# Optimization experiments

Measured on AMD Instinct MI355X. Metric: run time of the kernel, lower is better.

## Reference

```python
import jax, jax.numpy as jnp
import numpy as np

H_DIM = 1024
HEAD_SIZE = 1024


def setup_inputs() -> dict:
    key = jax.random.key(0)
    ks = jax.random.split(key, 7)
    s = 1.0 / np.sqrt(H_DIM)
    x = jax.random.normal(ks[0], (4, 4096, H_DIM), dtype=jnp.float32)
    Wq = jax.random.uniform(ks[1], (H_DIM, HEAD_SIZE), jnp.float32, -s, s)
    bq = jax.random.uniform(ks[2], (HEAD_SIZE,), jnp.float32, -s, s)
    Wk = jax.random.uniform(ks[3], (H_DIM, HEAD_SIZE), jnp.float32, -s, s)
    bk = jax.random.uniform(ks[4], (HEAD_SIZE,), jnp.float32, -s, s)
    Wv = jax.random.uniform(ks[5], (H_DIM, HEAD_SIZE), jnp.float32, -s, s)
    bv = jax.random.uniform(ks[6], (HEAD_SIZE,), jnp.float32, -s, s)
    return {"x": x, "Wq": Wq, "bq": bq, "Wk": Wk, "bk": bk, "Wv": Wv, "bv": bv}


def reference(x, Wq, bq, Wk, bk, Wv, bv):
    B, S, _ = x.shape
    q = x @ Wq + bq  # [B,S,hs]
    k = x @ Wk + bk
    v = x @ Wv + bv
    scores = jnp.einsum('bqd,bkd->bqk', q, k)  # [B,S,S]
    causal = jnp.tril(jnp.ones((S, S), dtype=bool))
    scores = jnp.where(causal, scores, -jnp.inf)
    # original divides after masking; -inf stays -inf so math is identical
    w = jax.nn.softmax(scores / jnp.sqrt(jnp.float32(HEAD_SIZE)), axis=-1)
    # dropout p=0.0 -> identity
    return jnp.einsum('bqk,bkd->bqd', w, v)
```

## Files before the change

kernel.cpp:

```cpp
#include <hip/hip_runtime.h>
#include <stdint.h>

typedef _Float16 f16;
typedef _Float16 v8h __attribute__((ext_vector_type(8)));
typedef _Float16 v4h __attribute__((ext_vector_type(4)));
typedef float v4f __attribute__((ext_vector_type(4)));

#define LOG2E 1.44269504088896340736f
#define PT 16384

__device__ __forceinline__ void gll16(const void* g, void* l) {
  __builtin_amdgcn_global_load_lds((__attribute__((address_space(1))) void*)g,
                                   (__attribute__((address_space(3))) void*)l,
                                   16, 0, 0);
}

__device__ __forceinline__ int xcd_swz(int p, int chunk) {
  return (p & 7) * chunk + (p >> 3);
}

__global__ void k_cvt_x(const float* __restrict__ x, f16* __restrict__ xh, int n4) {
  int i = blockIdx.x * blockDim.x + threadIdx.x;
  if (i >= n4) return;
  float4 v = ((const float4*)x)[i];
  v4h o;
  o[0] = (f16)v.x; o[1] = (f16)v.y; o[2] = (f16)v.z; o[3] = (f16)v.w;
  ((v4h*)xh)[i] = o;
}

__global__ void k_cvt_wt(const float* __restrict__ Wq, const float* __restrict__ Wk,
                         const float* __restrict__ Wv, f16* __restrict__ Wt) {
  __shared__ f16 tile[64][65];
  int z = blockIdx.z;
  const float* W = (z == 0) ? Wq : (z == 1) ? Wk : Wv;
  int k0 = blockIdx.y * 64, n0 = blockIdx.x * 64;
  int t = threadIdx.x;
  int r = t >> 4, c4 = t & 15;
  for (int i = 0; i < 4; ++i) {
    int row = r + i * 16;
    float4 v = *(const float4*)&W[(size_t)(k0 + row) * 1024 + n0 + c4 * 4];
    tile[c4 * 4 + 0][row] = (f16)v.x;
    tile[c4 * 4 + 1][row] = (f16)v.y;
    tile[c4 * 4 + 2][row] = (f16)v.z;
    tile[c4 * 4 + 3][row] = (f16)v.w;
  }
  __syncthreads();
  f16* out = Wt + (size_t)z * 1048576;
  for (int i = 0; i < 4; ++i) {
    int n = r + i * 16;
    v4h o;
    o[0] = tile[n][c4 * 4 + 0];
    o[1] = tile[n][c4 * 4 + 1];
    o[2] = tile[n][c4 * 4 + 2];
    o[3] = tile[n][c4 * 4 + 3];
    *(v4h*)&out[(size_t)(n0 + n) * 1024 + k0 + c4 * 4] = o;
  }
}

__global__ __launch_bounds__(512) void k_qkv(
    const f16* __restrict__ xh,
    const f16* __restrict__ Wt,
    const float* __restrict__ bq, const float* __restrict__ bk, const float* __restrict__ bv,
    f16* __restrict__ q, f16* __restrict__ k, f16* __restrict__ vT) {
  __shared__ __align__(16) f16 As[2][16384];
  __shared__ __align__(16) f16 Bs[2][16384];
  int p = blockIdx.x + 64 * (blockIdx.y + 4 * blockIdx.z);
  int l = xcd_swz(p, 96);
  int mt = l / 12;
  int rem = l - mt * 12;
  int z = rem >> 2, nt = rem & 3;
  int m0 = mt * 256, n0 = nt * 256;
  const f16* gA = xh + (size_t)m0 * 1024;
  const f16* gB = Wt + (size_t)z * 1048576 + (size_t)n0 * 1024;
  const float* bias = (z == 0) ? bq : (z == 1) ? bk : bv;
  int tid = threadIdx.x;
  int lane = tid & 63, wave = tid >> 6;
  int quad = lane >> 4, l15 = lane & 15;
  int wm = (wave >> 2) * 128, wn = (wave & 3) * 64;

  int soff[4], slds[4];
#pragma unroll
  for (int h = 0; h < 4; ++h) {
    int s = h * 512 + tid;
    int row = s >> 3;
    int c = (s & 7) ^ (row & 7);
    soff[h] = row * 1024 + c * 8;
    slds[h] = (h * 512 + wave * 64) * 8;
  }
  v4f acc[8][4] = {};
  v8h a[8], bfr[4];

#define QSTAGE(dst, g, kf) do {                                            \
    _Pragma("unroll") for (int h = 0; h < 4; ++h)                          \
      gll16((g) + soff[h] + (kf), &(dst)[slds[h]]);                        \
  } while (0)

#define QREAD(d, ks) do {                                                  \
    int sl = (((ks) * 4 + quad) ^ (l15 & 7)) * 8;                          \
    _Pragma("unroll") for (int i = 0; i < 8; ++i)                          \
      a[i] = *(const v8h*)&As[d][(wm + i * 16 + l15) * 64 + sl];           \
    _Pragma("unroll") for (int j = 0; j < 4; ++j)                          \
      bfr[j] = *(const v8h*)&Bs[d][(wn + j * 16 + l15) * 64 + sl];         \
  } while (0)

#define QMFMA() do {                                                       \
    __builtin_amdgcn_s_setprio(1);                                         \
    _Pragma("unroll") for (int i = 0; i < 8; ++i)                          \
      _Pragma("unroll") for (int j = 0; j < 4; ++j)                        \
        acc[i][j] = __builtin_amdgcn_mfma_f32_16x16x32_f16(a[i], bfr[j], acc[i][j], 0, 0, 0); \
    __builtin_amdgcn_s_setprio(0);                                         \
  } while (0)

  QSTAGE(As[0], gA, 0);
  QSTAGE(Bs[0], gB, 0);

#pragma unroll 1
  for (int it = 0; it < 7; ++it) {
    int k1 = (2 * it + 1) * 64, k2 = (2 * it + 2) * 64;
    QSTAGE(As[1], gA, k1);
    asm volatile("s_waitcnt vmcnt(4)" ::: "memory");
    __builtin_amdgcn_s_barrier();
    QREAD(0, 0); QMFMA();
    QREAD(0, 1);
    QSTAGE(Bs[1], gB, k1);
    QMFMA();
    __builtin_amdgcn_s_barrier();
    QSTAGE(As[0], gA, k2);
    asm volatile("s_waitcnt vmcnt(4)" ::: "memory");
    __builtin_amdgcn_s_barrier();
    QREAD(1, 0); QMFMA();
    QREAD(1, 1);
    QSTAGE(Bs[0], gB, k2);
    QMFMA();
    __builtin_amdgcn_s_barrier();
  }
  {
    int k1 = 15 * 64;
    QSTAGE(As[1], gA, k1);
    asm volatile("s_waitcnt vmcnt(4)" ::: "memory");
    __builtin_amdgcn_s_barrier();
    QREAD(0, 0); QMFMA();
    QREAD(0, 1);
    QSTAGE(Bs[1], gB, k1);
    QMFMA();
    __builtin_amdgcn_s_barrier();
    asm volatile("s_waitcnt vmcnt(0)" ::: "memory");
    __builtin_amdgcn_s_barrier();
    QREAD(1, 0); QMFMA();
    QREAD(1, 1); QMFMA();
  }
#undef QSTAGE
#undef QREAD
#undef QMFMA

  if (z < 2) {
    f16* outp = (z == 0) ? q : k;
    float scale = (z == 0) ? 0.03125f : 1.0f;
#pragma unroll
    for (int j = 0; j < 4; ++j) {
      int n = n0 + wn + j * 16 + l15;
      float bia = bias[n];
#pragma unroll
      for (int i = 0; i < 8; ++i) {
        int mb = m0 + wm + i * 16 + quad * 4;
#pragma unroll
        for (int r = 0; r < 4; ++r)
          outp[(size_t)(mb + r) * 1024 + n] = (f16)((acc[i][j][r] + bia) * scale);
      }
    }
  } else {
#pragma unroll
    for (int j = 0; j < 4; ++j) {
      int n = n0 + wn + j * 16 + l15;
      float bia = bias[n];
#pragma unroll
      for (int i = 0; i < 8; ++i) {
        int m = m0 + wm + i * 16 + quad * 4;
        int bb = m >> 12, s = m & 4095;
        v4h o;
#pragma unroll
        for (int r = 0; r < 4; ++r) o[r] = (f16)(acc[i][j][r] + bia);
        *(v4h*)&vT[((size_t)bb * 1024 + n) * 4096 + s] = o;
      }
    }
  }
}

__global__ void k_zero(float* __restrict__ p) {
  p[blockIdx.x * 256 + threadIdx.x] = 0.f;
}

__global__ __launch_bounds__(256) void k_sgemm(
    const f16* __restrict__ q, const f16* __restrict__ kmat,
    f16* __restrict__ P, float* __restrict__ rowsum, int b0) {
  __shared__ __align__(16) f16 As[128 * 32];
  __shared__ __align__(16) f16 Bs[128 * 32];
  int p = blockIdx.x + 528 * blockIdx.y;
  int l = xcd_swz(p, 132);
  int i = (l >= 528) ? l - 528 : l;
  int bb = (l >= 528) ? 1 : 0;
  int b = b0 * 2 + bb;
  int mt = (int)((sqrtf(8.f * i + 1.f) - 1.f) * 0.5f);
  while ((mt + 1) * (mt + 2) / 2 <= i) ++mt;
  while (mt * (mt + 1) / 2 > i) --mt;
  int nt = i - mt * (mt + 1) / 2;
  const f16* A = q + ((size_t)b * 4096 + (size_t)mt * 128) * 1024;
  const f16* B = kmat + ((size_t)b * 4096 + (size_t)nt * 128) * 1024;
  f16* Pt = P + (size_t)bb * 528 * PT + (size_t)i * PT;

  int tid = threadIdx.x;
  int lane = tid & 63, wave = tid >> 6;
  int quad = lane >> 4, l15 = lane & 15;
  int wm = (wave & 1) * 64, wn = (wave >> 1) * 64;
  v4f acc[4][4] = {};

  for (int kk = 0; kk < 1024; kk += 32) {
    __syncthreads();
    for (int h = 0; h < 2; ++h) {
      int s = h * 256 + tid;
      int row = s >> 2, pos = s & 3;
      int c = pos ^ (row & 3);
      gll16(&A[(size_t)row * 1024 + kk + c * 8], &As[(h * 256 + wave * 64) * 8]);
    }
    for (int h = 0; h < 2; ++h) {
      int s = h * 256 + tid;
      int row = s >> 2, pos = s & 3;
      int c = pos ^ (row & 3);
      gll16(&B[(size_t)row * 1024 + kk + c * 8], &Bs[(h * 256 + wave * 64) * 8]);
    }
    __syncthreads();
    v8h a[4], bf[4];
    for (int ii = 0; ii < 4; ++ii) {
      int rowa = wm + ii * 16 + l15;
      int pa = quad ^ (rowa & 3);
      a[ii] = *(const v8h*)&As[rowa * 32 + pa * 8];
      int rowb = wn + ii * 16 + l15;
      int pb = quad ^ (rowb & 3);
      bf[ii] = *(const v8h*)&Bs[rowb * 32 + pb * 8];
    }
    for (int ii = 0; ii < 4; ++ii)
      for (int j = 0; j < 4; ++j)
        acc[ii][j] = __builtin_amdgcn_mfma_f32_16x16x32_f16(a[ii], bf[j], acc[ii][j], 0, 0, 0);
  }

  bool diag = (nt == mt);
  float* rsb = rowsum + (size_t)b * 4096 + mt * 128;
  for (int ii = 0; ii < 4; ++ii) {
    int rl = wm + ii * 16 + quad * 4;
    for (int r = 0; r < 4; ++r) {
      int row_l = rl + r;
      float rs = 0.f;
      for (int j = 0; j < 4; ++j) {
        int col_l = wn + j * 16 + l15;
        float pv = __builtin_amdgcn_exp2f(acc[ii][j][r] * LOG2E);
        if (diag && col_l > row_l) pv = 0.f;
        Pt[(size_t)row_l * 128 + col_l] = (f16)pv;
        rs += pv;
      }
      rs += __shfl_xor(rs, 1, 64);
      rs += __shfl_xor(rs, 2, 64);
      rs += __shfl_xor(rs, 4, 64);
      rs += __shfl_xor(rs, 8, 64);
      if (l15 == 0) atomicAdd(&rsb[row_l], rs);
    }
  }
}

__global__ __launch_bounds__(256) void k_pv(
    const f16* __restrict__ P, const f16* __restrict__ vT,
    const float* __restrict__ rowsum, float* __restrict__ out, int b0) {
  __shared__ __align__(16) f16 As[2][8192];
  __shared__ __align__(16) f16 Bs[2][4096];
  int p = blockIdx.x + 16 * (blockIdx.y + 16 * blockIdx.z);
  int l = xcd_swz(p, 64);
  int dt = l & 15;
  int pr = (l >> 4) & 15;
  int bb = l >> 8;
  int b = b0 * 2 + bb;
  const f16* Pb = P + (size_t)bb * 528 * PT;
  const f16* Vb = vT + (size_t)b * 1024 * 4096;
  int tid = threadIdx.x;
  int lane = tid & 63, wave = tid >> 6;
  int quad = lane >> 4, l15 = lane & 15;
  int wm = (wave & 1) * 64, wn = (wave >> 1) * 32;

  int aoff[4], aslds[4];
#pragma unroll
  for (int h = 0; h < 4; ++h) {
    int s = h * 256 + tid;
    int row = s >> 3;
    int c = (s & 7) ^ (row & 7);
    aoff[h] = row * 128 + c * 8;
    aslds[h] = (h * 256 + wave * 64) * 8;
  }
  int boff[2], bslds[2];
#pragma unroll
  for (int h = 0; h < 2; ++h) {
    int s = h * 256 + tid;
    int row = s >> 3;
    int c = (s & 7) ^ (row & 7);
    boff[h] = (dt * 64 + row) * 4096 + c * 8;
    bslds[h] = (h * 256 + wave * 64) * 8;
  }
  v8h a[4], b_[2];

#define PSTAGE_A(d, Pt_, kc) do {                                          \
    _Pragma("unroll") for (int h = 0; h < 4; ++h)                          \
      gll16((Pt_) + aoff[h] + (kc), &As[d][aslds[h]]);                     \
  } while (0)
#define PSTAGE_B(d, koff) do {                                             \
    _Pragma("unroll") for (int h = 0; h < 2; ++h)                          \
      gll16(Vb + boff[h] + (koff), &Bs[d][bslds[h]]);                      \
  } while (0)
#define PREAD(d, ks) do {                                                  \
    int sl = (((ks) * 4 + quad) ^ (l15 & 7)) * 8;                          \
    _Pragma("unroll") for (int ii = 0; ii < 4; ++ii)                       \
      a[ii] = *(const v8h*)&As[d][(wm + ii * 16 + l15) * 64 + sl];         \
    _Pragma("unroll") for (int j = 0; j < 2; ++j)                          \
      b_[j] = *(const v8h*)&Bs[d][(wn + j * 16 + l15) * 64 + sl];          \
  } while (0)
#define PMFMA(acc_) do {                                                   \
    __builtin_amdgcn_s_setprio(1);                                         \
    _Pragma("unroll") for (int ii = 0; ii < 4; ++ii)                       \
      _Pragma("unroll") for (int j = 0; j < 2; ++j)                        \
        acc_[ii][j] = __builtin_amdgcn_mfma_f32_16x16x32_f16(a[ii], b_[j], acc_[ii][j], 0, 0, 0); \
    __builtin_amdgcn_s_setprio(0);                                         \
  } while (0)

  for (int half = 0; half < 2; ++half) {
    int mt = half ? (31 - pr) : pr;
    size_t ptri = (size_t)mt * (mt + 1) / 2;
    v4f acc[4][2] = {};
    PSTAGE_A(0, Pb + ptri * PT, 0);
    PSTAGE_B(0, 0);
#pragma unroll 1
    for (int i = 0; i < mt; ++i) {
      const f16* Pti = Pb + (ptri + i) * PT;
      const f16* Ptn = Pti + PT;
      PSTAGE_A(1, Pti, 64);
      asm volatile("s_waitcnt vmcnt(4)" ::: "memory");
      __builtin_amdgcn_s_barrier();
      PREAD(0, 0); PMFMA(acc);
      PREAD(0, 1);
      PSTAGE_B(1, i * 128 + 64);
      PMFMA(acc);
      __builtin_amdgcn_s_barrier();
      PSTAGE_A(0, Ptn, 0);
      asm volatile("s_waitcnt vmcnt(4)" ::: "memory");
      __builtin_amdgcn_s_barrier();
      PREAD(1, 0); PMFMA(acc);
      PREAD(1, 1);
      PSTAGE_B(0, (i + 1) * 128);
      PMFMA(acc);
      __builtin_amdgcn_s_barrier();
    }
    {
      const f16* Pti = Pb + (ptri + mt) * PT;
      PSTAGE_A(1, Pti, 64);
      asm volatile("s_waitcnt vmcnt(4)" ::: "memory");
      __builtin_amdgcn_s_barrier();
      PREAD(0, 0); PMFMA(acc);
      PREAD(0, 1);
      PSTAGE_B(1, mt * 128 + 64);
      PMFMA(acc);
      __builtin_amdgcn_s_barrier();
      asm volatile("s_waitcnt vmcnt(0)" ::: "memory");
      __builtin_amdgcn_s_barrier();
      PREAD(1, 0); PMFMA(acc);
      PREAD(1, 1); PMFMA(acc);
      __builtin_amdgcn_s_barrier();
    }
    const float* rsb = rowsum + (size_t)b * 4096 + mt * 128;
    float* ob = out + ((size_t)b * 4096 + (size_t)mt * 128) * 1024 + dt * 64;
    for (int ii = 0; ii < 4; ++ii) {
      int r0 = wm + ii * 16 + quad * 4;
      for (int r = 0; r < 4; ++r) {
        float inv = 1.0f / rsb[r0 + r];
        for (int j = 0; j < 2; ++j) {
          int cc = wn + j * 16 + l15;
          ob[(size_t)(r0 + r) * 1024 + cc] = acc[ii][j][r] * inv;
        }
      }
    }
  }
#undef PSTAGE_A
#undef PSTAGE_B
#undef PREAD
#undef PMFMA
}

extern "C" void kernel_launch(void* const* d_in, const int* in_sizes, int n_in,
                              void* d_out, int out_size, void* d_ws, size_t ws_size,
                              hipStream_t stream) {
  const float* x  = (const float*)d_in[0];
  const float* Wq = (const float*)d_in[1];
  const float* bq = (const float*)d_in[2];
  const float* Wk = (const float*)d_in[3];
  const float* bk = (const float*)d_in[4];
  const float* Wv = (const float*)d_in[5];
  const float* bv = (const float*)d_in[6];
  float* out = (float*)d_out;
  char* ws = (char*)d_ws;
  f16* xh = (f16*)(ws);
  f16* Wt = (f16*)(ws + 33554432);
  f16* q  = (f16*)(ws + 39845888);
  f16* k  = (f16*)(ws + 73400320);
  f16* vT = (f16*)(ws + 106954752);
  f16* P  = (f16*)(ws);
  float* rowsum = (float*)(ws + 34603008);

  k_cvt_x<<<16384, 256, 0, stream>>>(x, xh, 4194304);
  k_cvt_wt<<<dim3(16, 16, 3), 256, 0, stream>>>(Wq, Wk, Wv, Wt);
  k_qkv<<<dim3(64, 4, 3), 512, 0, stream>>>(xh, Wt, bq, bk, bv, q, k, vT);
  k_zero<<<64, 256, 0, stream>>>(rowsum);
  for (int bp = 0; bp < 2; ++bp) {
    k_sgemm<<<dim3(528, 2), 256, 0, stream>>>(q, k, P, rowsum, bp);
    k_pv<<<dim3(16, 16, 2), 256, 0, stream>>>(P, vT, rowsum, out, bp);
  }
}
```

Baseline: 472.4 us.

## Double-buffer LDS and widen K-step in QK^T score GEMM with staged prefetch

Rewrites the k_sgemm main loop to use two LDS buffers with a 64-wide K tile and an XOR swizzle over 8 chunks. Global-to-LDS loads for the next tile are issued while MFMAs run on the current one, with manual vmcnt waits, raw barriers and s_setprio around the MFMA bursts. This aims to hide load latency and halve the barrier count per K. In exchange LDS use grows fourfold (64KB), which may lower occupancy, and the hand-written waitcnt sequencing is fragile.

Measured after the change: 450.8 us. 4.6% less time.

```diff
diff --git a/kernel.cpp b/kernel.cpp
--- a/kernel.cpp
+++ b/kernel.cpp
@@ -193,8 +193,8 @@
 __global__ __launch_bounds__(256) void k_sgemm(
     const f16* __restrict__ q, const f16* __restrict__ kmat,
     f16* __restrict__ P, float* __restrict__ rowsum, int b0) {
-  __shared__ __align__(16) f16 As[128 * 32];
-  __shared__ __align__(16) f16 Bs[128 * 32];
+  __shared__ __align__(16) f16 As[2][8192];
+  __shared__ __align__(16) f16 Bs[2][8192];
   int p = blockIdx.x + 528 * blockIdx.y;
   int l = xcd_swz(p, 132);
   int i = (l >= 528) ? l - 528 : l;
@@ -212,36 +212,81 @@
   int lane = tid & 63, wave = tid >> 6;
   int quad = lane >> 4, l15 = lane & 15;
   int wm = (wave & 1) * 64, wn = (wave >> 1) * 64;
+
+  int soff[4], slds[4];
+#pragma unroll
+  for (int h = 0; h < 4; ++h) {
+    int s = h * 256 + tid;
+    int row = s >> 3;
+    int c = (s & 7) ^ (row & 7);
+    soff[h] = row * 1024 + c * 8;
+    slds[h] = (h * 256 + wave * 64) * 8;
+  }
   v4f acc[4][4] = {};
-
-  for (int kk = 0; kk < 1024; kk += 32) {
-    __syncthreads();
-    for (int h = 0; h < 2; ++h) {
-      int s = h * 256 + tid;
-      int row = s >> 2, pos = s & 3;
-      int c = pos ^ (row & 3);
-      gll16(&A[(size_t)row * 1024 + kk + c * 8], &As[(h * 256 + wave * 64) * 8]);
-    }
-    for (int h = 0; h < 2; ++h) {
-      int s = h * 256 + tid;
-      int row = s >> 2, pos = s & 3;
-      int c = pos ^ (row & 3);
-      gll16(&B[(size_t)row * 1024 + kk + c * 8], &Bs[(h * 256 + wave * 64) * 8]);
-    }
-    __syncthreads();
-    v8h a[4], bf[4];
-    for (int ii = 0; ii < 4; ++ii) {
-      int rowa = wm + ii * 16 + l15;
-      int pa = quad ^ (rowa & 3);
-      a[ii] = *(const v8h*)&As[rowa * 32 + pa * 8];
-      int rowb = wn + ii * 16 + l15;
-      int pb = quad ^ (rowb & 3);
-      bf[ii] = *(const v8h*)&Bs[rowb * 32 + pb * 8];
-    }
-    for (int ii = 0; ii < 4; ++ii)
-      for (int j = 0; j < 4; ++j)
-        acc[ii][j] = __builtin_amdgcn_mfma_f32_16x16x32_f16(a[ii], bf[j], acc[ii][j], 0, 0, 0);
-  }
+  v8h a[4], bf[4];
+
+#define SSTAGE(dst, g, kf) do {                                            \
+    _Pragma("unroll") for (int h = 0; h < 4; ++h)                          \
+      gll16((g) + soff[h] + (kf), &(dst)[slds[h]]);                        \
+  } while (0)
+
+#define SREAD(d, ks) do {                                                  \
+    int sl = (((ks) * 4 + quad) ^ (l15 & 7)) * 8;                          \
+    _Pragma("unroll") for (int ii = 0; ii < 4; ++ii)                       \
+      a[ii] = *(const v8h*)&As[d][(wm + ii * 16 + l15) * 64 + sl];         \
+    _Pragma("unroll") for (int j = 0; j < 4; ++j)                          \
+      bf[j] = *(const v8h*)&Bs[d][(wn + j * 16 + l15) * 64 + sl];          \
+  } while (0)
+
+#define SMFMA() do {                                                       \
+    __builtin_amdgcn_s_setprio(1);                                         \
+    _Pragma("unroll") for (int ii = 0; ii < 4; ++ii)                       \
+      _Pragma("unroll") for (int j = 0; j < 4; ++j)                        \
+        acc[ii][j] = __builtin_amdgcn_mfma_f32_16x16x32_f16(a[ii], bf[j], acc[ii][j], 0, 0, 0); \
+    __builtin_amdgcn_s_setprio(0);                                         \
+  } while (0)
+
+  SSTAGE(As[0], A, 0);
+  SSTAGE(Bs[0], B, 0);
+
+#pragma unroll 1
+  for (int it = 0; it < 7; ++it) {
+    int k1 = (2 * it + 1) * 64, k2 = (2 * it + 2) * 64;
+    SSTAGE(As[1], A, k1);
+    asm volatile("s_waitcnt vmcnt(4)" ::: "memory");
+    __builtin_amdgcn_s_barrier();
+    SREAD(0, 0); SMFMA();
+    SREAD(0, 1);
+    SSTAGE(Bs[1], B, k1);
+    SMFMA();
+    __builtin_amdgcn_s_barrier();
+    SSTAGE(As[0], A, k2);
+    asm volatile("s_waitcnt vmcnt(4)" ::: "memory");
+    __builtin_amdgcn_s_barrier();
+    SREAD(1, 0); SMFMA();
+    SREAD(1, 1);
+    SSTAGE(Bs[0], B, k2);
+    SMFMA();
+    __builtin_amdgcn_s_barrier();
+  }
+  {
+    int k1 = 15 * 64;
+    SSTAGE(As[1], A, k1);
+    asm volatile("s_waitcnt vmcnt(4)" ::: "memory");
+    __builtin_amdgcn_s_barrier();
+    SREAD(0, 0); SMFMA();
+    SREAD(0, 1);
+    SSTAGE(Bs[1], B, k1);
+    SMFMA();
+    __builtin_amdgcn_s_barrier();
+    asm volatile("s_waitcnt vmcnt(0)" ::: "memory");
+    __builtin_amdgcn_s_barrier();
+    SREAD(1, 0); SMFMA();
+    SREAD(1, 1); SMFMA();
+  }
+#undef SSTAGE
+#undef SREAD
+#undef SMFMA
 
   bool diag = (nt == mt);
   float* rsb = rowsum + (size_t)b * 4096 + mt * 128;
```
